# Kernel tuning notes

Measured on AMD Instinct MI355X. Metric: run time of the kernel, lower is better.

The kernel has to match this reference:

```python
import jax, jax.numpy as jnp
import numpy as np

N, E, D, L = 50000, 600000, 128, 2  # nodes, edges, hidden_dim, num_gnn_layers
NEG_SLOPE = 0.2  # PyG GATv2Conv default negative_slope


def setup_inputs() -> dict:
    key = jax.random.key(0)
    ks = jax.random.split(key, 10)
    s = 1.0 / np.sqrt(D)
    return {
        "x": jax.random.normal(ks[0], (N, D), jnp.float32),
        "edge_index": jax.random.randint(ks[1], (2, E), 0, N, dtype=jnp.int32),
        # per-layer GATv2 params (stacked over L layers)
        "Wl": jax.random.normal(ks[2], (L, D, D), jnp.float32) * s,  # lin_l (source)
        "bl": jnp.zeros((L, D), jnp.float32),
        "Wr": jax.random.normal(ks[3], (L, D, D), jnp.float32) * s,  # lin_r (target)
        "br": jnp.zeros((L, D), jnp.float32),
        "att": jax.random.normal(ks[4], (L, D), jnp.float32) * s,
        "bias": jnp.zeros((L, D), jnp.float32),
        # shared residual Linear
        "W_res": jax.random.normal(ks[5], (D, D), jnp.float32) * s,
        "b_res": jnp.zeros((D,), jnp.float32),
    }


def reference(x, edge_index, Wl, bl, Wr, br, att, bias, W_res, b_res):
    n = x.shape[0]
    # add self loops (PyG GATv2Conv default add_self_loops=True)
    loops = jnp.arange(n, dtype=edge_index.dtype)
    src = jnp.concatenate([edge_index[0], loops])  # source j (messages)
    dst = jnp.concatenate([edge_index[1], loops])  # target i (aggregation)

    def conv(h, i):
        xl = h @ Wl[i] + bl[i]  # [N, D] source transform
        xr = h @ Wr[i] + br[i]  # [N, D] target transform
        m = xl[src] + xr[dst]   # [E+N, D] gathered edge messages
        e = jnp.einsum('ed,d->e', jnp.where(m > 0, m, NEG_SLOPE * m), att[i])
        # segment softmax over incoming edges of each destination node
        emax = jax.lax.stop_gradient(jax.ops.segment_max(e, dst, num_segments=n))
        ex = jnp.exp(e - emax[dst])
        denom = jax.ops.segment_sum(ex, dst, num_segments=n)
        alpha = ex / (denom[dst] + 1e-16)
        out = jax.ops.segment_sum(alpha[:, None] * xl[src], dst, num_segments=n)
        return out + bias[i]

    for i in range(Wl.shape[0]):
        x = jax.nn.relu(conv(x, i) + x @ W_res + b_res)
    return x
```

## Files before the change

kernel.cpp:

```cpp
#include <hip/hip_runtime.h>
#include <math.h>


#define DIM 128
#define NEG_SLOPE 0.2f
#define TPW 4

typedef __attribute__((ext_vector_type(8))) short short8;
typedef __attribute__((ext_vector_type(4))) float floatx4;
typedef __attribute__((ext_vector_type(2))) float f32x2;

static __device__ __forceinline__ unsigned short f2b(float f) {
    unsigned u = __float_as_uint(f);
    unsigned r = (u + 0x7FFFu + ((u >> 16) & 1u)) >> 16;
    return (unsigned short)r;
}
static __device__ __forceinline__ f32x2 cvt2(unsigned u) {
    f32x2 r;
    r.x = __uint_as_float(u << 16);
    r.y = __uint_as_float(u & 0xffff0000u);
    return r;
}
static __device__ __forceinline__ f32x2 pk_add(f32x2 a, f32x2 b) {
    f32x2 d;
    asm("v_pk_add_f32 %0, %1, %2" : "=v"(d) : "v"(a), "v"(b));
    return d;
}
static __device__ __forceinline__ f32x2 pk_mul(f32x2 a, f32x2 b) {
    f32x2 d;
    asm("v_pk_mul_f32 %0, %1, %2" : "=v"(d) : "v"(a), "v"(b));
    return d;
}
static __device__ __forceinline__ f32x2 pk_fma(f32x2 a, f32x2 b, f32x2 c) {
    f32x2 d;
    asm("v_pk_fma_f32 %0, %1, %2, %3" : "=v"(d) : "v"(a), "v"(b), "v"(c));
    return d;
}
static __device__ __forceinline__ f32x2 absf2(f32x2 a) {
    f32x2 r;
    r.x = __builtin_fabsf(a.x);
    r.y = __builtin_fabsf(a.y);
    return r;
}

__global__ void k_count(const int* __restrict__ dst, int E, int* __restrict__ counts) {
    int k = blockIdx.x * blockDim.x + threadIdx.x;
    if (k < E) atomicAdd(&counts[dst[k]], 1);
}

__global__ void k_scan1(const int* __restrict__ counts, int n,
                        int* __restrict__ rowptr, int* __restrict__ bsum) {
    __shared__ int s[256];
    int tid = threadIdx.x;
    int i = blockIdx.x * 256 + tid;
    int v = (i < n) ? (counts[i] + 1) : 0;
    s[tid] = v;
    __syncthreads();
    for (int off = 1; off < 256; off <<= 1) {
        int t = (tid >= off) ? s[tid - off] : 0;
        __syncthreads();
        s[tid] += t;
        __syncthreads();
    }
    if (i < n) rowptr[i + 1] = s[tid];
    if (tid == 255) bsum[blockIdx.x] = s[255];
}

__global__ void k_scan2(int* __restrict__ bsum, int nb) {
    __shared__ int s[256];
    int tid = threadIdx.x;
    int v = (tid < nb) ? bsum[tid] : 0;
    s[tid] = v;
    __syncthreads();
    for (int off = 1; off < 256; off <<= 1) {
        int t = (tid >= off) ? s[tid - off] : 0;
        __syncthreads();
        s[tid] += t;
        __syncthreads();
    }
    if (tid < nb) bsum[tid] = s[tid];
}

__global__ void k_scan3(int* __restrict__ rowptr, const int* __restrict__ bsum,
                        int n, int* __restrict__ counts_to_cursors) {
    int i = blockIdx.x * 256 + threadIdx.x;
    if (i < n) {
        int add = (blockIdx.x > 0) ? bsum[blockIdx.x - 1] : 0;
        int cnt = counts_to_cursors[i] + 1;
        int v = rowptr[i + 1] + add;
        rowptr[i + 1] = v;
        counts_to_cursors[i] = v - cnt;
    }
    if (i == 0) rowptr[0] = 0;
}

__global__ void k_scatter(const int* __restrict__ src, const int* __restrict__ dst,
                          int E, int n, int* __restrict__ cur, int* __restrict__ srt) {
    int k = blockIdx.x * blockDim.x + threadIdx.x;
    int tot = E + n;
    if (k >= tot) return;
    int s, d;
    if (k < E) { s = src[k]; d = dst[k]; }
    else       { s = k - E;  d = s; }
    int p = atomicAdd(&cur[d], 1);
    srt[p] = s;
}

__global__ void k_pre(const float* __restrict__ Wl, const float* __restrict__ Wr,
                      const float* __restrict__ Wres, unsigned short* __restrict__ wfrag,
                      const float* __restrict__ h, unsigned short* __restrict__ hfrag,
                      int n, int ntiles) {
    int blk = blockIdx.x;
    if (blk < 48) {
        int idx = blk * 256 + threadIdx.x;
        int lane = idx & 63;
        int nr   = (idx >> 6) & 7;
        int ks   = (idx >> 9) & 3;
        int v    = idx >> 11;
        int sec = v % 3, l = v / 3;
        const float* W = (sec == 0) ? (Wl + l * DIM * DIM)
                       : (sec == 1) ? (Wr + l * DIM * DIM) : Wres;
        int nn = nr * 16 + (lane & 15);
        int k0 = ks * 32 + ((lane >> 4) << 3);
        ushort4 a, b;
        a.x = f2b(W[(k0 + 0) * DIM + nn]); a.y = f2b(W[(k0 + 1) * DIM + nn]);
        a.z = f2b(W[(k0 + 2) * DIM + nn]); a.w = f2b(W[(k0 + 3) * DIM + nn]);
        b.x = f2b(W[(k0 + 4) * DIM + nn]); b.y = f2b(W[(k0 + 5) * DIM + nn]);
        b.z = f2b(W[(k0 + 6) * DIM + nn]); b.w = f2b(W[(k0 + 7) * DIM + nn]);
        *(ushort4*)(wfrag + (size_t)idx * 8) = a;
        *(ushort4*)(wfrag + (size_t)idx * 8 + 4) = b;
    } else {
        int idx = (blk - 48) * 256 + threadIdx.x;
        if (idx >= ntiles * 256) return;
        int lane = idx & 63;
        int ks   = (idx >> 6) & 3;
        int tile = idx >> 8;
        int row  = tile * 16 + (lane & 15);
        int col0 = ks * 32 + ((lane >> 4) << 3);
        ushort4 a = {0, 0, 0, 0}, b = {0, 0, 0, 0};
        if (row < n) {
            float4 v0 = *(const float4*)(h + (size_t)row * DIM + col0);
            float4 v1 = *(const float4*)(h + (size_t)row * DIM + col0 + 4);
            a.x = f2b(v0.x); a.y = f2b(v0.y); a.z = f2b(v0.z); a.w = f2b(v0.w);
            b.x = f2b(v1.x); b.y = f2b(v1.y); b.z = f2b(v1.z); b.w = f2b(v1.w);
        }
        *(ushort4*)(hfrag + (size_t)idx * 8) = a;
        *(ushort4*)(hfrag + (size_t)idx * 8 + 4) = b;
    }
}

__global__ __launch_bounds__(256, 2) void k_gemm(
    const unsigned short* __restrict__ hfrag, const unsigned short* __restrict__ wfrag,
    const float* __restrict__ bl, const float* __restrict__ br, const float* __restrict__ bres,
    unsigned short* __restrict__ XLb, unsigned short* __restrict__ XRb,
    float* __restrict__ RES, int ntiles)
{
    int sec  = blockIdx.y;
    int lane = threadIdx.x & 63;
    int w    = threadIdx.x >> 6;

    const unsigned short* wbase = wfrag + (size_t)sec * (4 * 8 * 64 * 8);
    short8 bf[4][8];
#pragma unroll
    for (int ks = 0; ks < 4; ks++)
#pragma unroll
        for (int nr = 0; nr < 8; nr++)
            bf[ks][nr] = *(const short8*)(wbase + (((ks * 8 + nr) * 64 + lane) << 3));

    const float* bias = (sec == 0) ? bl : (sec == 1) ? br : bres;
    int colb = (lane >> 4) << 2;
    float4 bv[8];
#pragma unroll
    for (int nr = 0; nr < 8; nr++) bv[nr] = *(const float4*)(bias + nr * 16 + colb);

    int wid = blockIdx.x * 4 + w;
#pragma unroll
    for (int i = 0; i < TPW; i++) {
        int t = wid * TPW + i;
        if (t >= ntiles) break;
        short8 a[4];
#pragma unroll
        for (int ks = 0; ks < 4; ks++)
            a[ks] = *(const short8*)(hfrag + (((t * 4 + ks) * 64 + lane) << 3));
        floatx4 acc[8];
#pragma unroll
        for (int nr = 0; nr < 8; nr++) acc[nr] = (floatx4){0.f, 0.f, 0.f, 0.f};
#pragma unroll
        for (int ks = 0; ks < 4; ks++)
#pragma unroll
            for (int nr = 0; nr < 8; nr++)
                acc[nr] = __builtin_amdgcn_mfma_f32_16x16x32_bf16(bf[ks][nr], a[ks], acc[nr], 0, 0, 0);

        int row = t * 16 + (lane & 15);
        size_t rb = (size_t)row * DIM;
#pragma unroll
        for (int nr = 0; nr < 8; nr++) {
            float4 o;
            o.x = acc[nr][0] + bv[nr].x;
            o.y = acc[nr][1] + bv[nr].y;
            o.z = acc[nr][2] + bv[nr].z;
            o.w = acc[nr][3] + bv[nr].w;
            int col = nr * 16 + colb;
            if (sec == 2) {
                *(float4*)(RES + rb + col) = o;
            } else {
                ushort4 u;
                u.x = f2b(o.x); u.y = f2b(o.y); u.z = f2b(o.z); u.w = f2b(o.w);
                if (sec == 0) *(ushort4*)(XLb + rb + col) = u;
                else          *(ushort4*)(XRb + rb + col) = u;
            }
        }
    }
}

#define EDGE_P(K)                                                        \
    f32x2 v01_##K = cvt2(e##K.x), v23_##K = cvt2(e##K.y);                \
    float p##K;                                                          \
    {                                                                    \
        f32x2 t01 = pk_add(v01_##K, x01);                                \
        f32x2 t23 = pk_add(v23_##K, x23);                                \
        f32x2 pp = pk_mul(a6_01, t01);                                   \
        pp = pk_fma(a4_01, absf2(t01), pp);                              \
        pp = pk_fma(a6_23, t23, pp);                                     \
        pp = pk_fma(a4_23, absf2(t23), pp);                              \
        p##K = pp.x + pp.y;                                              \
    }

__global__ __launch_bounds__(256) void k_aggr(
    const unsigned short* __restrict__ XLb, const unsigned short* __restrict__ XRb,
    const float* __restrict__ RES, const float* __restrict__ att,
    const float* __restrict__ bias, const int* __restrict__ rowptr,
    const int* __restrict__ srt, float* __restrict__ outF,
    unsigned short* __restrict__ fragOut, int writeFrag, int n)
{
    int wave = threadIdx.x >> 6;
    int lane = threadIdx.x & 63;
    int node = blockIdx.x * 4 + wave;
    if (node >= n) return;
    int half = lane >> 5, sl = lane & 31;
    int d0 = sl << 2;

    float4 af = *(const float4*)(att + d0);
    f32x2 a6_01 = {0.6f * af.x, 0.6f * af.y}, a6_23 = {0.6f * af.z, 0.6f * af.w};
    f32x2 a4_01 = {0.4f * af.x, 0.4f * af.y}, a4_23 = {0.4f * af.z, 0.4f * af.w};

    uint2 xru = *(const uint2*)(XRb + (size_t)node * DIM + d0);
    f32x2 x01 = cvt2(xru.x), x23 = cvt2(xru.y);

    int beg = rowptr[node], end = rowptr[node + 1];
    int len = end - beg;
    int hl = (len + 1) >> 1;
    int sb = beg + half * hl;
    int se = half ? end : (beg + hl);

    const uint2* R = (const uint2*)XLb;

    f32x2 acc01 = {0.f, 0.f}, acc23 = {0.f, 0.f};
    float den = 0.f;

    for (int j = sb; j < se; j += 4) {
        int j1 = (j + 1 < se) ? j + 1 : j;
        int j2 = (j + 2 < se) ? j + 2 : j;
        int j3 = (j + 3 < se) ? j + 3 : j;
        int s0 = srt[j], s1 = srt[j1], s2 = srt[j2], s3 = srt[j3];
        uint2 e0 = R[(size_t)s0 * 32 + sl];
        uint2 e1 = R[(size_t)s1 * 32 + sl];
        uint2 e2 = R[(size_t)s2 * 32 + sl];
        uint2 e3 = R[(size_t)s3 * 32 + sl];
        EDGE_P(0) EDGE_P(1) EDGE_P(2) EDGE_P(3)
#pragma unroll
        for (int off = 16; off >= 1; off >>= 1) {
            p0 += __shfl_xor(p0, off);
            p1 += __shfl_xor(p1, off);
            p2 += __shfl_xor(p2, off);
            p3 += __shfl_xor(p3, off);
        }
        float w0 = __expf(fminf(p0, 80.f));
        float w1 = (j + 1 < se) ? __expf(fminf(p1, 80.f)) : 0.f;
        float w2 = (j + 2 < se) ? __expf(fminf(p2, 80.f)) : 0.f;
        float w3 = (j + 3 < se) ? __expf(fminf(p3, 80.f)) : 0.f;
        den += (w0 + w1) + (w2 + w3);
        acc01 = pk_fma((f32x2){w0, w0}, v01_0, acc01);
        acc23 = pk_fma((f32x2){w0, w0}, v23_0, acc23);
        acc01 = pk_fma((f32x2){w1, w1}, v01_1, acc01);
        acc23 = pk_fma((f32x2){w1, w1}, v23_1, acc23);
        acc01 = pk_fma((f32x2){w2, w2}, v01_2, acc01);
        acc23 = pk_fma((f32x2){w2, w2}, v23_2, acc23);
        acc01 = pk_fma((f32x2){w3, w3}, v01_3, acc01);
        acc23 = pk_fma((f32x2){w3, w3}, v23_3, acc23);
    }

    den     += __shfl_xor(den, 32);
    acc01.x += __shfl_xor(acc01.x, 32);
    acc01.y += __shfl_xor(acc01.y, 32);
    acc23.x += __shfl_xor(acc23.x, 32);
    acc23.y += __shfl_xor(acc23.y, 32);
    if (half) return;

    float inv = 1.f / (den + 1e-16f);
    float4 r4 = *(const float4*)(RES + (size_t)node * DIM + d0);
    float4 b4 = *(const float4*)(bias + d0);
    float4 o;
    o.x = fmaxf(acc01.x * inv + b4.x + r4.x, 0.f);
    o.y = fmaxf(acc01.y * inv + b4.y + r4.y, 0.f);
    o.z = fmaxf(acc23.x * inv + b4.z + r4.z, 0.f);
    o.w = fmaxf(acc23.y * inv + b4.w + r4.w, 0.f);

    if (writeFrag) {
        int tile = node >> 4;
        int ks = sl >> 3;
        int li = (node & 15) + (((sl >> 1) & 3) << 4);
        int j0 = (sl & 1) << 2;
        ushort4 u;
        u.x = f2b(o.x); u.y = f2b(o.y); u.z = f2b(o.z); u.w = f2b(o.w);
        *(ushort4*)(fragOut + ((size_t)((tile * 4 + ks) * 64 + li) << 3) + j0) = u;
    } else {
        *(float4*)(outF + (size_t)node * DIM + d0) = o;
    }
}

extern "C" void kernel_launch(void* const* d_in, const int* in_sizes, int n_in,
                              void* d_out, int out_size, void* d_ws, size_t ws_size,
                              hipStream_t stream) {
    const float* x    = (const float*)d_in[0];
    const int*   ei   = (const int*)d_in[1];
    const float* Wl   = (const float*)d_in[2];
    const float* bl   = (const float*)d_in[3];
    const float* Wr   = (const float*)d_in[4];
    const float* br   = (const float*)d_in[5];
    const float* att  = (const float*)d_in[6];
    const float* bias = (const float*)d_in[7];
    const float* Wres = (const float*)d_in[8];
    const float* bres = (const float*)d_in[9];

    int n = in_sizes[0] / DIM;
    int E = in_sizes[1] / 2;
    int ntiles = (n + 15) >> 4;
    const int* srcIdx = ei;
    const int* dstIdx = ei + E;

    float* resb = (float*)d_ws;
    unsigned short* xlb   = (unsigned short*)(resb + (size_t)n * DIM);
    unsigned short* xrb   = xlb + (size_t)n * DIM;
    unsigned short* hfrag = xrb + (size_t)n * DIM;
    unsigned short* wfrag = hfrag + (size_t)ntiles * 16 * DIM;
    int* rowptr = (int*)(wfrag + 2 * 3 * DIM * DIM);
    int* tmpc   = rowptr + (n + 1);
    int* srt    = tmpc + n;
    int* bsum   = srt + (E + n + 8);

    int nb1 = (n + 255) / 256;

    k_pre<<<48 + ntiles, 256, 0, stream>>>(Wl, Wr, Wres, wfrag, x, hfrag, n, ntiles);
    hipMemsetAsync(tmpc, 0, (size_t)n * sizeof(int), stream);
    k_count<<<(E + 255) / 256, 256, 0, stream>>>(dstIdx, E, tmpc);
    k_scan1<<<nb1, 256, 0, stream>>>(tmpc, n, rowptr, bsum);
    k_scan2<<<1, 256, 0, stream>>>(bsum, nb1);
    k_scan3<<<nb1, 256, 0, stream>>>(rowptr, bsum, n, tmpc);
    k_scatter<<<(E + n + 255) / 256, 256, 0, stream>>>(srcIdx, dstIdx, E, n, tmpc, srt);

    int gx = (ntiles + 4 * TPW - 1) / (4 * TPW);
    for (int l = 0; l < 2; l++) {
        dim3 g(gx, 3);
        k_gemm<<<g, 256, 0, stream>>>(hfrag, wfrag + (size_t)l * 3 * 4 * 8 * 64 * 8,
                                      bl + (size_t)l * DIM, br + (size_t)l * DIM, bres,
                                      xlb, xrb, resb, ntiles);
        k_aggr<<<(n + 3) / 4, 256, 0, stream>>>(xlb, xrb, resb, att + (size_t)l * DIM,
                                                bias + (size_t)l * DIM, rowptr, srt,
                                                (float*)d_out, hfrag, (l == 0) ? 1 : 0, n);
    }
}
```

Before: 223.3 us.

## Process four edges per wave with 16-lane groups and software-prefetch gathers

Restructures the aggregation kernel so each wave splits into four 16-lane groups, each handling one edge per iteration with 16-byte (8 bf16) gathers instead of two halves doing four edges each with 8-byte loads. The next edge's source row is prefetched while the current one is computed, and the attention scale is folded with log2(e) so exp2 replaces exp. The per-edge score reduction shrinks to four shuffle steps, but the final cross-group reduction is larger and there is a per-iteration index clamp.

```diff
diff --git a/kernel.cpp b/kernel.cpp
--- a/kernel.cpp
+++ b/kernel.cpp
@@ -213,19 +213,6 @@
     }
 }
 
-#define EDGE_P(K)                                                        \
-    f32x2 v01_##K = cvt2(e##K.x), v23_##K = cvt2(e##K.y);                \
-    float p##K;                                                          \
-    {                                                                    \
-        f32x2 t01 = pk_add(v01_##K, x01);                                \
-        f32x2 t23 = pk_add(v23_##K, x23);                                \
-        f32x2 pp = pk_mul(a6_01, t01);                                   \
-        pp = pk_fma(a4_01, absf2(t01), pp);                              \
-        pp = pk_fma(a6_23, t23, pp);                                     \
-        pp = pk_fma(a4_23, absf2(t23), pp);                              \
-        p##K = pp.x + pp.y;                                              \
-    }
-
 __global__ __launch_bounds__(256) void k_aggr(
     const unsigned short* __restrict__ XLb, const unsigned short* __restrict__ XRb,
     const float* __restrict__ RES, const float* __restrict__ att,
@@ -237,85 +224,110 @@
     int lane = threadIdx.x & 63;
     int node = blockIdx.x * 4 + wave;
     if (node >= n) return;
-    int half = lane >> 5, sl = lane & 31;
-    int d0 = sl << 2;
-
-    float4 af = *(const float4*)(att + d0);
-    f32x2 a6_01 = {0.6f * af.x, 0.6f * af.y}, a6_23 = {0.6f * af.z, 0.6f * af.w};
-    f32x2 a4_01 = {0.4f * af.x, 0.4f * af.y}, a4_23 = {0.4f * af.z, 0.4f * af.w};
-
-    uint2 xru = *(const uint2*)(XRb + (size_t)node * DIM + d0);
-    f32x2 x01 = cvt2(xru.x), x23 = cvt2(xru.y);
+    int g = lane >> 4;
+    int i = lane & 15;
+    int d0 = i << 3;
+
+    const float S6 = 0.6f * 1.44269504089f;
+    const float S4 = 0.4f * 1.44269504089f;
+    float4 af0 = *(const float4*)(att + d0);
+    float4 af1 = *(const float4*)(att + d0 + 4);
+    f32x2 a6[4] = {{S6 * af0.x, S6 * af0.y}, {S6 * af0.z, S6 * af0.w},
+                   {S6 * af1.x, S6 * af1.y}, {S6 * af1.z, S6 * af1.w}};
+    f32x2 a4[4] = {{S4 * af0.x, S4 * af0.y}, {S4 * af0.z, S4 * af0.w},
+                   {S4 * af1.x, S4 * af1.y}, {S4 * af1.z, S4 * af1.w}};
+
+    uint4 xu = *(const uint4*)(XRb + (size_t)node * DIM + d0);
+    f32x2 xv0 = cvt2(xu.x), xv1 = cvt2(xu.y), xv2 = cvt2(xu.z), xv3 = cvt2(xu.w);
 
     int beg = rowptr[node], end = rowptr[node + 1];
-    int len = end - beg;
-    int hl = (len + 1) >> 1;
-    int sb = beg + half * hl;
-    int se = half ? end : (beg + hl);
-
-    const uint2* R = (const uint2*)XLb;
-
-    f32x2 acc01 = {0.f, 0.f}, acc23 = {0.f, 0.f};
+    const uint4* R = (const uint4*)XLb;
+
+    f32x2 acc0 = {0.f, 0.f}, acc1 = {0.f, 0.f}, acc2 = {0.f, 0.f}, acc3 = {0.f, 0.f};
     float den = 0.f;
 
-    for (int j = sb; j < se; j += 4) {
-        int j1 = (j + 1 < se) ? j + 1 : j;
-        int j2 = (j + 2 < se) ? j + 2 : j;
-        int j3 = (j + 3 < se) ? j + 3 : j;
-        int s0 = srt[j], s1 = srt[j1], s2 = srt[j2], s3 = srt[j3];
-        uint2 e0 = R[(size_t)s0 * 32 + sl];
-        uint2 e1 = R[(size_t)s1 * 32 + sl];
-        uint2 e2 = R[(size_t)s2 * 32 + sl];
-        uint2 e3 = R[(size_t)s3 * 32 + sl];
-        EDGE_P(0) EDGE_P(1) EDGE_P(2) EDGE_P(3)
-#pragma unroll
-        for (int off = 16; off >= 1; off >>= 1) {
-            p0 += __shfl_xor(p0, off);
-            p1 += __shfl_xor(p1, off);
-            p2 += __shfl_xor(p2, off);
-            p3 += __shfl_xor(p3, off);
-        }
-        float w0 = __expf(fminf(p0, 80.f));
-        float w1 = (j + 1 < se) ? __expf(fminf(p1, 80.f)) : 0.f;
-        float w2 = (j + 2 < se) ? __expf(fminf(p2, 80.f)) : 0.f;
-        float w3 = (j + 3 < se) ? __expf(fminf(p3, 80.f)) : 0.f;
-        den += (w0 + w1) + (w2 + w3);
-        acc01 = pk_fma((f32x2){w0, w0}, v01_0, acc01);
-        acc23 = pk_fma((f32x2){w0, w0}, v23_0, acc23);
-        acc01 = pk_fma((f32x2){w1, w1}, v01_1, acc01);
-        acc23 = pk_fma((f32x2){w1, w1}, v23_1, acc23);
-        acc01 = pk_fma((f32x2){w2, w2}, v01_2, acc01);
-        acc23 = pk_fma((f32x2){w2, w2}, v23_2, acc23);
-        acc01 = pk_fma((f32x2){w3, w3}, v01_3, acc01);
-        acc23 = pk_fma((f32x2){w3, w3}, v23_3, acc23);
-    }
-
-    den     += __shfl_xor(den, 32);
-    acc01.x += __shfl_xor(acc01.x, 32);
-    acc01.y += __shfl_xor(acc01.y, 32);
-    acc23.x += __shfl_xor(acc23.x, 32);
-    acc23.y += __shfl_xor(acc23.y, 32);
-    if (half) return;
+    int jj = beg + g;
+    int s0 = srt[(jj < end) ? jj : (end - 1)];
+    uint4 u = R[((size_t)s0 << 4) + i];
+
+    for (int jb = beg; jb < end; jb += 4) {
+        int jjn = jb + 4 + g;
+        int sn = srt[(jjn < end) ? jjn : (end - 1)];
+        uint4 un = R[((size_t)sn << 4) + i];
+
+        f32x2 v0 = cvt2(u.x), v1 = cvt2(u.y), v2 = cvt2(u.z), v3 = cvt2(u.w);
+        f32x2 t0 = pk_add(v0, xv0);
+        f32x2 t1 = pk_add(v1, xv1);
+        f32x2 t2 = pk_add(v2, xv2);
+        f32x2 t3 = pk_add(v3, xv3);
+        f32x2 pp = pk_mul(a6[0], t0);
+        pp = pk_fma(a6[1], t1, pp);
+        pp = pk_fma(a6[2], t2, pp);
+        pp = pk_fma(a6[3], t3, pp);
+        pp = pk_fma(a4[0], absf2(t0), pp);
+        pp = pk_fma(a4[1], absf2(t1), pp);
+        pp = pk_fma(a4[2], absf2(t2), pp);
+        pp = pk_fma(a4[3], absf2(t3), pp);
+        float p = pp.x + pp.y;
+        p += __shfl_xor(p, 1);
+        p += __shfl_xor(p, 2);
+        p += __shfl_xor(p, 4);
+        p += __shfl_xor(p, 8);
+        float w = __builtin_exp2f(fminf(p, 120.f));
+        w = (jb + g < end) ? w : 0.f;
+        den += w;
+        f32x2 wp = {w, w};
+        acc0 = pk_fma(wp, v0, acc0);
+        acc1 = pk_fma(wp, v1, acc1);
+        acc2 = pk_fma(wp, v2, acc2);
+        acc3 = pk_fma(wp, v3, acc3);
+
+        u = un;
+        jj = jjn;
+    }
+
+#pragma unroll
+    for (int off = 16; off <= 32; off <<= 1) {
+        den    += __shfl_xor(den, off);
+        acc0.x += __shfl_xor(acc0.x, off);
+        acc0.y += __shfl_xor(acc0.y, off);
+        acc1.x += __shfl_xor(acc1.x, off);
+        acc1.y += __shfl_xor(acc1.y, off);
+        acc2.x += __shfl_xor(acc2.x, off);
+        acc2.y += __shfl_xor(acc2.y, off);
+        acc3.x += __shfl_xor(acc3.x, off);
+        acc3.y += __shfl_xor(acc3.y, off);
+    }
+    if (g) return;
 
     float inv = 1.f / (den + 1e-16f);
-    float4 r4 = *(const float4*)(RES + (size_t)node * DIM + d0);
-    float4 b4 = *(const float4*)(bias + d0);
-    float4 o;
-    o.x = fmaxf(acc01.x * inv + b4.x + r4.x, 0.f);
-    o.y = fmaxf(acc01.y * inv + b4.y + r4.y, 0.f);
-    o.z = fmaxf(acc23.x * inv + b4.z + r4.z, 0.f);
-    o.w = fmaxf(acc23.y * inv + b4.w + r4.w, 0.f);
+    float4 r0 = *(const float4*)(RES + (size_t)node * DIM + d0);
+    float4 r1 = *(const float4*)(RES + (size_t)node * DIM + d0 + 4);
+    float4 b0 = *(const float4*)(bias + d0);
+    float4 b1 = *(const float4*)(bias + d0 + 4);
+    float of[8];
+    of[0] = fmaxf(acc0.x * inv + b0.x + r0.x, 0.f);
+    of[1] = fmaxf(acc0.y * inv + b0.y + r0.y, 0.f);
+    of[2] = fmaxf(acc1.x * inv + b0.z + r0.z, 0.f);
+    of[3] = fmaxf(acc1.y * inv + b0.w + r0.w, 0.f);
+    of[4] = fmaxf(acc2.x * inv + b1.x + r1.x, 0.f);
+    of[5] = fmaxf(acc2.y * inv + b1.y + r1.y, 0.f);
+    of[6] = fmaxf(acc3.x * inv + b1.z + r1.z, 0.f);
+    of[7] = fmaxf(acc3.y * inv + b1.w + r1.w, 0.f);
 
     if (writeFrag) {
-        int tile = node >> 4;
-        int ks = sl >> 3;
-        int li = (node & 15) + (((sl >> 1) & 3) << 4);
-        int j0 = (sl & 1) << 2;
-        ushort4 u;
-        u.x = f2b(o.x); u.y = f2b(o.y); u.z = f2b(o.z); u.w = f2b(o.w);
-        *(ushort4*)(fragOut + ((size_t)((tile * 4 + ks) * 64 + li) << 3) + j0) = u;
+        int tile = node >> 4, r16 = node & 15;
+        unsigned short* p0 = fragOut +
+            ((size_t)((tile * 4 + (i >> 2)) * 64 + r16 + ((i & 3) << 4)) << 3);
+        ushort4 ua, ub;
+        ua.x = f2b(of[0]); ua.y = f2b(of[1]); ua.z = f2b(of[2]); ua.w = f2b(of[3]);
+        ub.x = f2b(of[4]); ub.y = f2b(of[5]); ub.z = f2b(of[6]); ub.w = f2b(of[7]);
+        *(ushort4*)p0 = ua;
+        *(ushort4*)(p0 + 4) = ub;
     } else {
-        *(float4*)(outF + (size_t)node * DIM + d0) = o;
+        float* po = outF + (size_t)node * DIM + d0;
+        *(float4*)po = make_float4(of[0], of[1], of[2], of[3]);
+        *(float4*)(po + 4) = make_float4(of[4], of[5], of[6], of[7]);
     }
 }
 
```

After: 237.2 us. 1.06x slower.
